# Performance work log

Hardware: AMD Instinct MI355X
Metric: run time of the kernel (lower is better)

Reference implementation:

```python
import jax, jax.numpy as jnp
import numpy as np

NUM_RELATIONS = 8
DROP_P = 0.2


def rgcn_layer(x, W, root, b, edge_index, edge_type, num_relations):
    # x: [N,F], W: [R,F,O], root: [F,O], b: [O]
    # edge_index: [2,E] (row 0 = source, row 1 = target), edge_type: [E]
    src, dst = edge_index[0], edge_index[1]
    N = x.shape[0]
    O = W.shape[2]
    # Transform all nodes under every relation once: [R,N,O]
    transformed = jnp.einsum('nf,rfo->rno', x, W)
    msg = transformed[edge_type, src]  # [E,O] gather per edge
    # mean aggregation per relation: per-(relation,target) in-degree
    deg = jnp.zeros((num_relations, N), x.dtype).at[edge_type, dst].add(1.0)
    coef = (1.0 / jnp.clip(deg, 1.0))[edge_type, dst]  # [E]
    agg = jnp.zeros((N, O), x.dtype).at[dst].add(msg * coef[:, None])
    return agg + x @ root + b


def setup_inputs() -> dict:
    key = jax.random.key(0)
    ks = jax.random.split(key, 10)
    N, E, F, H, O, R = 50000, 400000, 128, 128, 64, NUM_RELATIONS
    x = jax.random.normal(ks[0], (N, F), jnp.float32)
    edge_index = jax.random.randint(ks[1], (2, E), 0, N, jnp.int64)
    edge_type = jax.random.randint(ks[2], (E,), 0, R, jnp.int64)
    s = 1.0 / np.sqrt(F)
    W1 = jax.random.normal(ks[3], (R, F, H), jnp.float32) * s
    root1 = jax.random.normal(ks[4], (F, H), jnp.float32) * s
    b1 = jnp.zeros((H,), jnp.float32)
    sh = 1.0 / np.sqrt(H)
    W2 = jax.random.normal(ks[5], (R, H, O), jnp.float32) * sh
    root2 = jax.random.normal(ks[6], (H, O), jnp.float32) * sh
    b2 = jnp.zeros((O,), jnp.float32)
    # inverted dropout mask (training mode, p=0.2), precomputed for determinism
    keep = jax.random.bernoulli(ks[7], 1.0 - DROP_P, (N, H))
    drop_mask = keep.astype(jnp.float32) / (1.0 - DROP_P)
    return {"x": x, "edge_index": edge_index, "edge_type": edge_type,
            "W1": W1, "root1": root1, "b1": b1,
            "W2": W2, "root2": root2, "b2": b2, "drop_mask": drop_mask}


def reference(x, edge_index, edge_type, W1, root1, b1, W2, root2, b2, drop_mask):
    h = rgcn_layer(x, W1, root1, b1, edge_index, edge_type, NUM_RELATIONS)
    h = jax.nn.relu(h) * drop_mask  # fused relu + dropout
    out = rgcn_layer(h, W2, root2, b2, edge_index, edge_type, NUM_RELATIONS)
    return out
```

## Files before the change

kernel.cpp:

```cpp
#include <hip/hip_runtime.h>
#include <hip/hip_bf16.h>
#include <stdint.h>

typedef __attribute__((ext_vector_type(8))) short bf16x8;
typedef __attribute__((ext_vector_type(4))) float f32x4;

__device__ __forceinline__ unsigned f2bf(float f){
  unsigned u = __builtin_bit_cast(unsigned, f);
  return (u + 0x7FFFu + ((u >> 16) & 1u)) >> 16;
}
__device__ __forceinline__ float bf2f(unsigned s){
  unsigned u = s << 16; return __builtin_bit_cast(float, u);
}
__device__ __forceinline__ void add8(float* a, uint4 g){
  a[0] += bf2f(g.x & 0xFFFFu); a[1] += bf2f(g.x >> 16);
  a[2] += bf2f(g.y & 0xFFFFu); a[3] += bf2f(g.y >> 16);
  a[4] += bf2f(g.z & 0xFFFFu); a[5] += bf2f(g.z >> 16);
  a[6] += bf2f(g.w & 0xFFFFu); a[7] += bf2f(g.w >> 16);
}
__device__ __forceinline__ void stage16(const void* g, void* l){
  __builtin_amdgcn_global_load_lds((const __attribute__((address_space(1))) void*)g,
                                   (__attribute__((address_space(3))) void*)l, 16, 0, 0);
}

__global__ void k_combo(const float* __restrict__ x,
                        const float* __restrict__ W1, const float* __restrict__ r1,
                        const float* __restrict__ W2, const float* __restrict__ r2,
                        const int* __restrict__ ei, const int* __restrict__ et,
                        short* __restrict__ Wt1, short* __restrict__ Wt2,
                        uint2* __restrict__ xb, int* __restrict__ degr,
                        int N, int E, int WB, int XB){
  int b = blockIdx.x, tid = threadIdx.x;
  if (b < WB){
    int t = b * 256 + tid;
    if (t < 128 * 1152){
      int o = t / 1152, ka = t - o * 1152, ph = ka >> 7, k = ka & 127;
      int kk = k >> 5, q = (k >> 3) & 3, j = k & 7;
      float v = (ph < 8) ? W1[(ph * 128 + k) * 128 + o] : r1[k * 128 + o];
      Wt1[(((ph * 4 + kk) * 4 + q) * 128 + o) * 8 + j] = (short)f2bf(v);
    } else if (t < 128 * 1152 + 64 * 1152){
      int t2 = t - 128 * 1152;
      int o = t2 / 1152, ka = t2 - o * 1152, ph = ka >> 7, k = ka & 127;
      int kk = k >> 5, q = (k >> 3) & 3, j = k & 7;
      float v = (ph < 8) ? W2[(ph * 128 + k) * 64 + o] : r2[k * 64 + o];
      Wt2[(((ph * 4 + kk) * 4 + q) * 64 + o) * 8 + j] = (short)f2bf(v);
    }
  } else if (b < WB + XB){
    int t = (b - WB) * 256 + tid;
    if (t < N * 32){
      float4 v = reinterpret_cast<const float4*>(x)[t];
      uint2 o;
      o.x = f2bf(v.x) | (f2bf(v.y) << 16);
      o.y = f2bf(v.z) | (f2bf(v.w) << 16);
      xb[t] = o;
    }
  } else {
    int e = (b - WB - XB) * 256 + tid;
    if (e < E){
      unsigned dst = (unsigned)ei[E + e];
      int rel = et[e] & 7;
      if (dst < (unsigned)N) atomicAdd(&degr[rel * N + dst], 1);
    }
  }
}

__global__ void k_scan(const int* __restrict__ cnt, int* __restrict__ gcnt,
                       int* __restrict__ offs, unsigned* __restrict__ pmeta, int M){
  __shared__ int s[256];
  __shared__ int sbase;
  int i = blockIdx.x * 256 + threadIdx.x;
  int v = (i < M) ? cnt[i] : 0;
  s[threadIdx.x] = v; __syncthreads();
  for (int d = 1; d < 256; d <<= 1){
    int t = (threadIdx.x >= d) ? s[threadIdx.x - d] : 0;
    __syncthreads();
    s[threadIdx.x] += t;
    __syncthreads();
  }
  if (threadIdx.x == 255) sbase = atomicAdd(gcnt, s[255]);
  __syncthreads();
  if (i < M){
    int off = sbase + s[threadIdx.x] - v;
    offs[i] = off;
    int c = v; if (c > 4095) c = 4095;
    pmeta[i] = (unsigned)off | ((unsigned)c << 20);
  }
}

__global__ void k_fill(const int* __restrict__ ei, const int* __restrict__ et,
                       const int* __restrict__ offs, int* __restrict__ fill,
                       unsigned short* __restrict__ idx, int E, int N){
  int e = blockIdx.x * 256 + threadIdx.x;
  if (e >= E) return;
  unsigned src = (unsigned)ei[e];
  unsigned dst = (unsigned)ei[E + e];
  int rel = et[e] & 7;
  if (dst < (unsigned)N){
    int key = rel * N + (int)dst;
    int p = atomicAdd(&fill[key], 1);
    idx[offs[key] + p] = (unsigned short)src;
  }
}

template<int NF, int MODE>
__global__ __launch_bounds__(256, 4)
void k_fused(const short* __restrict__ feat, const unsigned* __restrict__ pmeta,
             const unsigned short* __restrict__ idx2, const short* __restrict__ Wt,
             const float* __restrict__ bias, const float* __restrict__ mask,
             void* __restrict__ outp, int N){
  constexpr int BN = NF * 16;
  constexpr int NPW = NF / 4;
  __shared__ char sA[8 * 16 * 256];
  int tid = threadIdx.x, lane = tid & 63, wave = tid >> 6;
  int row0 = blockIdx.x * 16;
  int r = tid >> 4, l = tid & 15;
  int dstj = row0 + r;
  bool vd = dstj < N;
  int c = l ^ (r & 7);

  unsigned m[8];
  #pragma unroll
  for (int ph = 0; ph < 8; ph++) m[ph] = vd ? pmeta[ph * N + dstj] : 0u;
  int s0[8];
  #pragma unroll
  for (int ph = 0; ph < 8; ph++){
    int cnt = (int)(m[ph] >> 20), base = (int)(m[ph] & 0xFFFFFu);
    s0[ph] = (cnt > 0) ? (int)idx2[base] : N;
  }
  #pragma unroll
  for (int ph = 0; ph < 8; ph++)
    stage16(feat + (size_t)s0[ph] * 128 + c * 8, sA + ph * 4096 + wave * 1024);

  uint4 g1[8];
  #pragma unroll
  for (int ph = 0; ph < 8; ph++){
    int cnt = (int)(m[ph] >> 20), base = (int)(m[ph] & 0xFFFFFu);
    if (cnt > 1)
      g1[ph] = *reinterpret_cast<const uint4*>(
          feat + (size_t)(int)idx2[base + 1] * 128 + c * 8);
  }

  int r16 = lane & 15, q = lane >> 4;
  int rsafe = row0 + r16; if (rsafe > N) rsafe = N;
  bf16x8 avr[4];
  #pragma unroll
  for (int kk = 0; kk < 4; kk++)
    avr[kk] = *reinterpret_cast<const bf16x8*>(
        feat + (size_t)rsafe * 128 + kk * 32 + q * 8);

  asm volatile("s_waitcnt vmcnt(0)" ::: "memory");

  #pragma unroll
  for (int ph = 0; ph < 8; ph++){
    int cnt = (int)(m[ph] >> 20), base = (int)(m[ph] & 0xFFFFFu);
    if (cnt > 1){
      uint4 v = *reinterpret_cast<uint4*>(sA + ph * 4096 + r * 256 + l * 16);
      float a[8];
      a[0]=bf2f(v.x&0xFFFFu); a[1]=bf2f(v.x>>16);
      a[2]=bf2f(v.y&0xFFFFu); a[3]=bf2f(v.y>>16);
      a[4]=bf2f(v.z&0xFFFFu); a[5]=bf2f(v.z>>16);
      a[6]=bf2f(v.w&0xFFFFu); a[7]=bf2f(v.w>>16);
      add8(a, g1[ph]);
      for (int i = 2; i < cnt; i++){
        int s = (int)idx2[base + i];
        uint4 gi = *reinterpret_cast<const uint4*>(feat + (size_t)s * 128 + c * 8);
        add8(a, gi);
      }
      float inv = 1.0f / (float)cnt;
      uint4 o;
      o.x = f2bf(a[0]*inv) | (f2bf(a[1]*inv) << 16);
      o.y = f2bf(a[2]*inv) | (f2bf(a[3]*inv) << 16);
      o.z = f2bf(a[4]*inv) | (f2bf(a[5]*inv) << 16);
      o.w = f2bf(a[6]*inv) | (f2bf(a[7]*inv) << 16);
      *reinterpret_cast<uint4*>(sA + ph * 4096 + r * 256 + l * 16) = o;
    }
  }
  __syncthreads();

  f32x4 acc[NPW];
  f32x4 z = {0.f, 0.f, 0.f, 0.f};
  #pragma unroll
  for (int nn = 0; nn < NPW; nn++) acc[nn] = z;
  int obase = wave * NPW * 16 + r16;

  #pragma unroll
  for (int ph = 0; ph < 9; ph++){
    #pragma unroll
    for (int kk = 0; kk < 4; kk++){
      bf16x8 av;
      if (ph < 8){
        int ch = ((kk * 4 + q) ^ (r16 & 7)) << 4;
        av = *reinterpret_cast<const bf16x8*>(sA + ph * 4096 + r16 * 256 + ch);
      } else {
        av = avr[kk];
      }
      #pragma unroll
      for (int nn = 0; nn < NPW; nn++){
        bf16x8 bv = *reinterpret_cast<const bf16x8*>(
            Wt + ((size_t)((ph * 4 + kk) * 4 + q) * BN + obase + nn * 16) * 8);
        acc[nn] = __builtin_amdgcn_mfma_f32_16x16x32_bf16(av, bv, acc[nn], 0, 0, 0);
      }
    }
  }

  #pragma unroll
  for (int nn = 0; nn < NPW; nn++){
    int col = obase + nn * 16;
    float bv = bias[col];
    #pragma unroll
    for (int j = 0; j < 4; j++){
      int row = row0 + (q << 2) + j;
      if (row < N){
        float v = acc[nn][j] + bv;
        if (MODE == 1){
          v = fmaxf(v, 0.f) * mask[(size_t)row * 128 + col];
          reinterpret_cast<short*>(outp)[(size_t)row * 128 + col] = (short)f2bf(v);
        } else {
          reinterpret_cast<float*>(outp)[(size_t)row * BN + col] = v;
        }
      }
    }
  }
}

extern "C" void kernel_launch(void* const* d_in, const int* in_sizes, int n_in,
                              void* d_out, int out_size, void* d_ws, size_t ws_size,
                              hipStream_t stream){
  const float* x    = (const float*)d_in[0];
  const int*   ei   = (const int*)d_in[1];
  const int*   et   = (const int*)d_in[2];
  const float* W1   = (const float*)d_in[3];
  const float* r1   = (const float*)d_in[4];
  const float* b1   = (const float*)d_in[5];
  const float* W2   = (const float*)d_in[6];
  const float* r2   = (const float*)d_in[7];
  const float* b2   = (const float*)d_in[8];
  const float* mask = (const float*)d_in[9];
  int N = in_sizes[0] / 128;
  int E = in_sizes[2];
  int M8 = 8 * N;

  char* ws = (char*)d_ws;
  short*    xb    = (short*)(ws + 0);
  short*    hb    = (short*)(ws + 12800512);
  short*    Wt1   = (short*)(ws + 25601024);
  short*    Wt2   = (short*)(ws + 25895936);
  int*      degr  = (int*)(ws + 26043392);
  int*      fill  = (int*)(ws + 27643392);
  int*      gcnt  = (int*)(ws + 29243392);
  int*      offs2 = (int*)(ws + 29243456);
  unsigned* pmeta = (unsigned*)(ws + 30843456);
  unsigned short* idx2 = (unsigned short*)(ws + 32443456);
  if (ws_size < (size_t)32443456 + (size_t)E * 2 + 64) return;

  hipMemsetAsync(degr, 0, (size_t)M8 * 8 + 64, stream);
  hipMemsetAsync(xb + (size_t)N * 128, 0, 256, stream);
  hipMemsetAsync(hb + (size_t)N * 128, 0, 256, stream);

  int WB = (128*1152 + 64*1152 + 255) / 256;
  int XB = (N * 32 + 255) / 256;
  int EB = (E + 255) / 256;
  int NB = (M8 + 255) / 256;
  k_combo<<<WB + XB + EB, 256, 0, stream>>>(x, W1, r1, W2, r2, ei, et,
                                            Wt1, Wt2, (uint2*)xb, degr, N, E, WB, XB);
  k_scan<<<NB, 256, 0, stream>>>(degr, gcnt, offs2, pmeta, M8);
  k_fill<<<EB, 256, 0, stream>>>(ei, et, offs2, fill, idx2, E, N);

  int G = (N + 15) / 16;
  k_fused<8, 1><<<G, 256, 0, stream>>>(xb, pmeta, idx2, Wt1, b1, mask, hb, N);
  k_fused<4, 2><<<G, 256, 0, stream>>>(hb, pmeta, idx2, Wt2, b2, nullptr, d_out, N);
}
```

Measured before the change: 284.6 us.

## Process 32 destination rows per block to reuse weight fragments across two MFMA tiles

```diff
diff --git a/kernel.cpp b/kernel.cpp
--- a/kernel.cpp
+++ b/kernel.cpp
@@ -103,102 +103,115 @@
 }
 
 template<int NF, int MODE>
-__global__ __launch_bounds__(256, 4)
+__global__ __launch_bounds__(256, 2)
 void k_fused(const short* __restrict__ feat, const unsigned* __restrict__ pmeta,
              const unsigned short* __restrict__ idx2, const short* __restrict__ Wt,
              const float* __restrict__ bias, const float* __restrict__ mask,
              void* __restrict__ outp, int N){
   constexpr int BN = NF * 16;
   constexpr int NPW = NF / 4;
-  __shared__ char sA[8 * 16 * 256];
+  __shared__ char sA[8 * 32 * 256];
   int tid = threadIdx.x, lane = tid & 63, wave = tid >> 6;
-  int row0 = blockIdx.x * 16;
+  int row0 = blockIdx.x * 32;
   int r = tid >> 4, l = tid & 15;
-  int dstj = row0 + r;
-  bool vd = dstj < N;
   int c = l ^ (r & 7);
-
-  unsigned m[8];
-  #pragma unroll
-  for (int ph = 0; ph < 8; ph++) m[ph] = vd ? pmeta[ph * N + dstj] : 0u;
-  int s0[8];
+  int rA = row0 + r, rB = row0 + 16 + r;
+  bool vA = rA < N, vB = rB < N;
+
+  unsigned mA[8], mB[8];
   #pragma unroll
   for (int ph = 0; ph < 8; ph++){
-    int cnt = (int)(m[ph] >> 20), base = (int)(m[ph] & 0xFFFFFu);
-    s0[ph] = (cnt > 0) ? (int)idx2[base] : N;
-  }
-  #pragma unroll
-  for (int ph = 0; ph < 8; ph++)
-    stage16(feat + (size_t)s0[ph] * 128 + c * 8, sA + ph * 4096 + wave * 1024);
-
-  uint4 g1[8];
+    mA[ph] = vA ? pmeta[ph * N + rA] : 0u;
+    mB[ph] = vB ? pmeta[ph * N + rB] : 0u;
+  }
+  int s0A[8], s1A[8], s0B[8], s1B[8];
   #pragma unroll
   for (int ph = 0; ph < 8; ph++){
-    int cnt = (int)(m[ph] >> 20), base = (int)(m[ph] & 0xFFFFFu);
-    if (cnt > 1)
-      g1[ph] = *reinterpret_cast<const uint4*>(
-          feat + (size_t)(int)idx2[base + 1] * 128 + c * 8);
+    int ca = (int)(mA[ph] >> 20), ba = (int)(mA[ph] & 0xFFFFFu);
+    s0A[ph] = (ca > 0) ? (int)idx2[ba] : N;
+    s1A[ph] = (ca > 1) ? (int)idx2[ba + 1] : N;
+    int cb = (int)(mB[ph] >> 20), bb = (int)(mB[ph] & 0xFFFFFu);
+    s0B[ph] = (cb > 0) ? (int)idx2[bb] : N;
+    s1B[ph] = (cb > 1) ? (int)idx2[bb + 1] : N;
+  }
+  #pragma unroll
+  for (int ph = 0; ph < 8; ph++){
+    stage16(feat + (size_t)s0A[ph] * 128 + c * 8, sA + ph * 8192 + wave * 1024);
+    stage16(feat + (size_t)s0B[ph] * 128 + c * 8, sA + ph * 8192 + 4096 + wave * 1024);
   }
 
   int r16 = lane & 15, q = lane >> 4;
-  int rsafe = row0 + r16; if (rsafe > N) rsafe = N;
-  bf16x8 avr[4];
-  #pragma unroll
-  for (int kk = 0; kk < 4; kk++)
-    avr[kk] = *reinterpret_cast<const bf16x8*>(
-        feat + (size_t)rsafe * 128 + kk * 32 + q * 8);
+  int rsA = row0 + r16;      if (rsA > N) rsA = N;
+  int rsB = row0 + 16 + r16; if (rsB > N) rsB = N;
+  bf16x8 avrA[4], avrB[4];
+  #pragma unroll
+  for (int kk = 0; kk < 4; kk++){
+    avrA[kk] = *reinterpret_cast<const bf16x8*>(feat + (size_t)rsA * 128 + kk * 32 + q * 8);
+    avrB[kk] = *reinterpret_cast<const bf16x8*>(feat + (size_t)rsB * 128 + kk * 32 + q * 8);
+  }
 
   asm volatile("s_waitcnt vmcnt(0)" ::: "memory");
 
   #pragma unroll
-  for (int ph = 0; ph < 8; ph++){
-    int cnt = (int)(m[ph] >> 20), base = (int)(m[ph] & 0xFFFFFu);
-    if (cnt > 1){
-      uint4 v = *reinterpret_cast<uint4*>(sA + ph * 4096 + r * 256 + l * 16);
-      float a[8];
-      a[0]=bf2f(v.x&0xFFFFu); a[1]=bf2f(v.x>>16);
-      a[2]=bf2f(v.y&0xFFFFu); a[3]=bf2f(v.y>>16);
-      a[4]=bf2f(v.z&0xFFFFu); a[5]=bf2f(v.z>>16);
-      a[6]=bf2f(v.w&0xFFFFu); a[7]=bf2f(v.w>>16);
-      add8(a, g1[ph]);
-      for (int i = 2; i < cnt; i++){
-        int s = (int)idx2[base + i];
-        uint4 gi = *reinterpret_cast<const uint4*>(feat + (size_t)s * 128 + c * 8);
-        add8(a, gi);
-      }
-      float inv = 1.0f / (float)cnt;
-      uint4 o;
-      o.x = f2bf(a[0]*inv) | (f2bf(a[1]*inv) << 16);
-      o.y = f2bf(a[2]*inv) | (f2bf(a[3]*inv) << 16);
-      o.z = f2bf(a[4]*inv) | (f2bf(a[5]*inv) << 16);
-      o.w = f2bf(a[6]*inv) | (f2bf(a[7]*inv) << 16);
-      *reinterpret_cast<uint4*>(sA + ph * 4096 + r * 256 + l * 16) = o;
+  for (int half = 0; half < 2; half++){
+    const unsigned* m  = half ? mB  : mA;
+    const int*      s1 = half ? s1B : s1A;
+    int ldsr = half ? (16 + r) : r;
+    #pragma unroll
+    for (int ph = 0; ph < 8; ph++){
+      int cnt = (int)(m[ph] >> 20), base = (int)(m[ph] & 0xFFFFFu);
+      if (cnt > 1){
+        uint4 v = *reinterpret_cast<uint4*>(sA + ph * 8192 + ldsr * 256 + l * 16);
+        float a[8];
+        a[0]=bf2f(v.x&0xFFFFu); a[1]=bf2f(v.x>>16);
+        a[2]=bf2f(v.y&0xFFFFu); a[3]=bf2f(v.y>>16);
+        a[4]=bf2f(v.z&0xFFFFu); a[5]=bf2f(v.z>>16);
+        a[6]=bf2f(v.w&0xFFFFu); a[7]=bf2f(v.w>>16);
+        uint4 g1 = *reinterpret_cast<const uint4*>(feat + (size_t)s1[ph] * 128 + c * 8);
+        add8(a, g1);
+        for (int i = 2; i < cnt; i++){
+          int s = (int)idx2[base + i];
+          uint4 gi = *reinterpret_cast<const uint4*>(feat + (size_t)s * 128 + c * 8);
+          add8(a, gi);
+        }
+        float inv = 1.0f / (float)cnt;
+        uint4 o;
+        o.x = f2bf(a[0]*inv) | (f2bf(a[1]*inv) << 16);
+        o.y = f2bf(a[2]*inv) | (f2bf(a[3]*inv) << 16);
+        o.z = f2bf(a[4]*inv) | (f2bf(a[5]*inv) << 16);
+        o.w = f2bf(a[6]*inv) | (f2bf(a[7]*inv) << 16);
+        *reinterpret_cast<uint4*>(sA + ph * 8192 + ldsr * 256 + l * 16) = o;
+      }
     }
   }
   __syncthreads();
 
-  f32x4 acc[NPW];
+  f32x4 acc[2][NPW];
   f32x4 z = {0.f, 0.f, 0.f, 0.f};
   #pragma unroll
-  for (int nn = 0; nn < NPW; nn++) acc[nn] = z;
+  for (int m = 0; m < 2; m++)
+    #pragma unroll
+    for (int nn = 0; nn < NPW; nn++) acc[m][nn] = z;
   int obase = wave * NPW * 16 + r16;
 
   #pragma unroll
   for (int ph = 0; ph < 9; ph++){
     #pragma unroll
     for (int kk = 0; kk < 4; kk++){
-      bf16x8 av;
+      bf16x8 avA, avB;
       if (ph < 8){
         int ch = ((kk * 4 + q) ^ (r16 & 7)) << 4;
-        av = *reinterpret_cast<const bf16x8*>(sA + ph * 4096 + r16 * 256 + ch);
+        avA = *reinterpret_cast<const bf16x8*>(sA + ph * 8192 + r16 * 256 + ch);
+        avB = *reinterpret_cast<const bf16x8*>(sA + ph * 8192 + 4096 + r16 * 256 + ch);
       } else {
-        av = avr[kk];
+        avA = avrA[kk]; avB = avrB[kk];
       }
       #pragma unroll
       for (int nn = 0; nn < NPW; nn++){
         bf16x8 bv = *reinterpret_cast<const bf16x8*>(
             Wt + ((size_t)((ph * 4 + kk) * 4 + q) * BN + obase + nn * 16) * 8);
-        acc[nn] = __builtin_amdgcn_mfma_f32_16x16x32_bf16(av, bv, acc[nn], 0, 0, 0);
+        acc[0][nn] = __builtin_amdgcn_mfma_f32_16x16x32_bf16(avA, bv, acc[0][nn], 0, 0, 0);
+        acc[1][nn] = __builtin_amdgcn_mfma_f32_16x16x32_bf16(avB, bv, acc[1][nn], 0, 0, 0);
       }
     }
   }
@@ -208,15 +221,18 @@
     int col = obase + nn * 16;
     float bv = bias[col];
     #pragma unroll
-    for (int j = 0; j < 4; j++){
-      int row = row0 + (q << 2) + j;
-      if (row < N){
-        float v = acc[nn][j] + bv;
-        if (MODE == 1){
-          v = fmaxf(v, 0.f) * mask[(size_t)row * 128 + col];
-          reinterpret_cast<short*>(outp)[(size_t)row * 128 + col] = (short)f2bf(v);
-        } else {
-          reinterpret_cast<float*>(outp)[(size_t)row * BN + col] = v;
+    for (int m = 0; m < 2; m++){
+      #pragma unroll
+      for (int j = 0; j < 4; j++){
+        int row = row0 + m * 16 + (q << 2) + j;
+        if (row < N){
+          float v = acc[m][nn][j] + bv;
+          if (MODE == 1){
+            v = fmaxf(v, 0.f) * mask[(size_t)row * 128 + col];
+            reinterpret_cast<short*>(outp)[(size_t)row * 128 + col] = (short)f2bf(v);
+          } else {
+            reinterpret_cast<float*>(outp)[(size_t)row * BN + col] = v;
+          }
         }
       }
     }
@@ -266,7 +282,7 @@
   k_scan<<<NB, 256, 0, stream>>>(degr, gcnt, offs2, pmeta, M8);
   k_fill<<<EB, 256, 0, stream>>>(ei, et, offs2, fill, idx2, E, N);
 
-  int G = (N + 15) / 16;
+  int G = (N + 31) / 32;
   k_fused<8, 1><<<G, 256, 0, stream>>>(xb, pmeta, idx2, Wt1, b1, mask, hb, N);
   k_fused<4, 2><<<G, 256, 0, stream>>>(hb, pmeta, idx2, Wt2, b2, nullptr, d_out, N);
 }
```

Result: slower. 332.7 us (+16.9%).
